# Optimization experiments

Hardware: AMD Instinct MI355X
Metric: run time of the kernel (lower is better)

Reference implementation:

```python
import jax, jax.numpy as jnp
import numpy as np

D_K = 64
NEG_INF = -1.0e9


def setup_inputs() -> dict:
    key = jax.random.key(0)
    kq, kk, kv = jax.random.split(key, 3)
    B, H, S, D = 2, 16, 2048, D_K
    Q = jax.random.normal(kq, (B, H, S, D), dtype=jnp.float32)
    K = jax.random.normal(kk, (B, H, S, D), dtype=jnp.float32)
    V = jax.random.normal(kv, (B, H, S, D), dtype=jnp.float32)
    # causal mask: True where attention is DISALLOWED (strict upper triangle)
    attn_mask = jnp.triu(jnp.ones((S, S), dtype=bool), k=1)
    return {"Q": Q, "K": K, "V": V, "attn_mask": attn_mask}


def reference(Q, K, V, attn_mask):
    # scores = Q @ (K / sqrt(d_k))^T  -> [B,H,S,S]
    scale = 1.0 / np.sqrt(D_K).astype(np.float32)
    scores = jnp.einsum("bhqd,bhkd->bhqk", Q, K * scale)
    scores = jnp.where(attn_mask, NEG_INF, scores)  # masked_fill_(mask, -1e9)
    attn = jax.nn.softmax(scores, axis=-1)
    context = jnp.einsum("bhqk,bhkd->bhqd", attn, V)
    return (context, attn)
```

## Files before the change

### kernel.cpp

```cpp
#include <hip/hip_runtime.h>

constexpr int S_LEN = 2048;
constexpr int D_K   = 64;
constexpr int N_BH  = 32;
constexpr int KB    = 64;
constexpr int PLP   = 80;

typedef __attribute__((ext_vector_type(8))) short short8;
typedef __attribute__((ext_vector_type(4))) float f32x4;
typedef unsigned short ushort_t;

__device__ __forceinline__ unsigned short f2bf(float f) {
    unsigned int u = __builtin_bit_cast(unsigned int, f);
    u += 0x7fffu + ((u >> 16) & 1u);
    return (unsigned short)(u >> 16);
}
__device__ __forceinline__ float bf2f(unsigned short h) {
    unsigned int u = ((unsigned int)h) << 16;
    return __builtin_bit_cast(float, u);
}

__global__ __launch_bounds__(256)
void prep_k(const float* __restrict__ K, ushort_t* __restrict__ Kws) {
    const int idx = blockIdx.x * 256 + threadIdx.x;
    const float4* src = (const float4*)K + (size_t)idx * 2;
    float4 a = src[0], b = src[1];
    float x[8] = {a.x, a.y, a.z, a.w, b.x, b.y, b.z, b.w};
    short8 o;
    #pragma unroll
    for (int j = 0; j < 8; ++j) o[j] = (short)f2bf(x[j] * 0.125f);
    *(short8*)(Kws + (size_t)idx * 8) = o;
}

__global__ __launch_bounds__(256)
void prep_v(const float* __restrict__ V, ushort_t* __restrict__ Vws) {
    const int gid = blockIdx.x * 256 + threadIdx.x;
    const int u   = gid & 511;
    const int bc  = gid >> 9;
    const int c   = bc & 31;
    const int bh  = bc >> 5;
    const int kg  = u >> 6;
    const int d   = u & 63;
    const float* vp = V + ((size_t)bh * S_LEN + c * KB + kg * 8) * D_K + d;
    short8 o;
    #pragma unroll
    for (int i = 0; i < 8; ++i) o[i] = (short)f2bf(vp[(size_t)i * D_K]);
    *(short8*)(Vws + ((size_t)(bh * 32 + c) * D_K + d) * KB + kg * 8) = o;
}

__global__ __launch_bounds__(512, 4)
void sdpa_main(const float* __restrict__ Q, const ushort_t* __restrict__ Kws,
               const ushort_t* __restrict__ Vws, float* __restrict__ out)
{
    __shared__ __align__(16) ushort_t Kbuf[2][4096];
    __shared__ __align__(16) ushort_t Vbuf[2][4096];
    __shared__ __align__(16) ushort_t Plds[8][16 * PLP];

    const int tid = threadIdx.x;
    const int w   = tid >> 6;
    const int l   = tid & 63;
    const int lr  = l & 15;
    const int lh  = l >> 4;

    const int b    = blockIdx.x;
    const int s    = b >> 8;
    const int cidx = b & 255;
    const int rmap = cidx & 7;
    const int bh   = cidx >> 3;
    const int qblk = s ? (15 - rmap) : rmap;
    const int q0   = qblk * 128;
    const int qw   = q0 + w * 16;
    const int nch  = 2 * (qblk + 1);

    float* ctx_out  = out;
    float* attn_out = out + (size_t)N_BH * S_LEN * D_K;

    short8 qhi[2], qlo[2];
    {
        const float* qrow = Q + ((size_t)bh * S_LEN + qw + lr) * D_K;
        #pragma unroll
        for (int ds = 0; ds < 2; ++ds) {
            const float4* p4 = (const float4*)(qrow + ds * 32 + lh * 8);
            float4 a = p4[0], bq = p4[1];
            float x[8] = {a.x, a.y, a.z, a.w, bq.x, bq.y, bq.z, bq.w};
            short8 hi, lo;
            #pragma unroll
            for (int j = 0; j < 8; ++j) {
                unsigned short h = f2bf(x[j]);
                hi[j] = (short)h;
                lo[j] = (short)f2bf(x[j] - bf2f(h));
            }
            qhi[ds] = hi; qlo[ds] = lo;
        }
    }

    const short8* Kt  = (const short8*)(Kws + (size_t)bh * S_LEN * D_K);
    const short8* Vt8 = (const short8*)(Vws + (size_t)bh * 32 * 4096);

    const int wrow  = tid >> 3;
    const int wcol  = (tid & 7) << 4;
    const int wphys = wrow * 128 + (wcol ^ ((wrow & 7) << 4));

    const int rsw = (lr & 7) << 4;

    float inv_[4];
    {
        float sum[4] = {0.f, 0.f, 0.f, 0.f};
        short8 kst = Kt[tid];
        *(short8*)((char*)&Kbuf[0][0] + wphys) = kst;
        __syncthreads();
        for (int c = 0; c < nch; ++c) {
            if (c + 1 < nch) kst = Kt[(c + 1) * 512 + tid];
            const char* Kb = (const char*)&Kbuf[c & 1][0];
            #pragma unroll
            for (int nt = 0; nt < 4; ++nt) {
                f32x4 acc = {0.f, 0.f, 0.f, 0.f};
                #pragma unroll
                for (int ks = 0; ks < 2; ++ks) {
                    short8 bk = *(const short8*)(Kb + (nt * 16 + lr) * 128 + ((ks * 64 + lh * 16) ^ rsw));
                    acc = __builtin_amdgcn_mfma_f32_16x16x32_bf16(qhi[ks], bk, acc, 0, 0, 0);
                    acc = __builtin_amdgcn_mfma_f32_16x16x32_bf16(qlo[ks], bk, acc, 0, 0, 0);
                }
                const int kg = c * KB + nt * 16 + lr;
                #pragma unroll
                for (int rr = 0; rr < 4; ++rr) {
                    if (kg <= qw + lh * 4 + rr)
                        sum[rr] += __expf(fminf(acc[rr], 60.f));
                }
            }
            if (c + 1 < nch) *(short8*)((char*)&Kbuf[(c + 1) & 1][0] + wphys) = kst;
            __syncthreads();
        }
        #pragma unroll
        for (int rr = 0; rr < 4; ++rr) {
            float t = sum[rr];
            t += __shfl_xor(t, 1);
            t += __shfl_xor(t, 2);
            t += __shfl_xor(t, 4);
            t += __shfl_xor(t, 8);
            inv_[rr] = 1.f / t;
        }
    }

    f32x4 ctx[4];
    #pragma unroll
    for (int nt = 0; nt < 4; ++nt) ctx[nt] = (f32x4){0.f, 0.f, 0.f, 0.f};

    {
        short8 kst = Kt[tid], vst = Vt8[tid];
        *(short8*)((char*)&Kbuf[0][0] + wphys) = kst;
        *(short8*)((char*)&Vbuf[0][0] + wphys) = vst;
        __syncthreads();
        for (int c = 0; c < nch; ++c) {
            if (c + 1 < nch) {
                kst = Kt[(c + 1) * 512 + tid];
                vst = Vt8[(c + 1) * 512 + tid];
            }
            const char* Kb = (const char*)&Kbuf[c & 1][0];
            const char* Vb = (const char*)&Vbuf[c & 1][0];

            #pragma unroll
            for (int nt = 0; nt < 4; ++nt) {
                f32x4 acc = {0.f, 0.f, 0.f, 0.f};
                #pragma unroll
                for (int ks = 0; ks < 2; ++ks) {
                    short8 bk = *(const short8*)(Kb + (nt * 16 + lr) * 128 + ((ks * 64 + lh * 16) ^ rsw));
                    acc = __builtin_amdgcn_mfma_f32_16x16x32_bf16(qhi[ks], bk, acc, 0, 0, 0);
                    acc = __builtin_amdgcn_mfma_f32_16x16x32_bf16(qlo[ks], bk, acc, 0, 0, 0);
                }
                const int kg = c * KB + nt * 16 + lr;
                #pragma unroll
                for (int rr = 0; rr < 4; ++rr) {
                    const int qg = qw + lh * 4 + rr;
                    float p = (kg <= qg) ? __expf(fminf(acc[rr], 60.f)) * inv_[rr] : 0.f;
                    attn_out[((size_t)bh * S_LEN + qg) * S_LEN + kg] = p;
                    Plds[w][(lh * 4 + rr) * PLP + nt * 16 + lr] = f2bf(p);
                }
            }

            #pragma unroll
            for (int ks = 0; ks < 2; ++ks) {
                short8 pa = *(const short8*)&Plds[w][lr * PLP + ks * 32 + lh * 8];
                #pragma unroll
                for (int nt = 0; nt < 4; ++nt) {
                    short8 vb = *(const short8*)(Vb + (nt * 16 + lr) * 128 + ((ks * 64 + lh * 16) ^ rsw));
                    ctx[nt] = __builtin_amdgcn_mfma_f32_16x16x32_bf16(pa, vb, ctx[nt], 0, 0, 0);
                }
            }

            if (c + 1 < nch) {
                *(short8*)((char*)&Kbuf[(c + 1) & 1][0] + wphys) = kst;
                *(short8*)((char*)&Vbuf[(c + 1) & 1][0] + wphys) = vst;
            }
            __syncthreads();
        }
    }

    #pragma unroll
    for (int nt = 0; nt < 4; ++nt)
        #pragma unroll
        for (int rr = 0; rr < 4; ++rr)
            ctx_out[((size_t)bh * S_LEN + qw + lh * 4 + rr) * D_K + nt * 16 + lr] = ctx[nt][rr];

    const int k0 = nch * KB;
    if (k0 < S_LEN) {
        const float4 z = {0.f, 0.f, 0.f, 0.f};
        for (int rr = 0; rr < 128; ++rr) {
            float* rowp = attn_out + ((size_t)bh * S_LEN + q0 + rr) * S_LEN;
            for (int k = k0 + tid * 4; k < S_LEN; k += 512 * 4)
                *(float4*)(rowp + k) = z;
        }
    }
}

constexpr int LDP = 72;

__global__ __launch_bounds__(256)
void sdpa_fused_v1(const float* __restrict__ Q, const float* __restrict__ K,
                   const float* __restrict__ V, float* __restrict__ out)
{
    __shared__ __align__(16) unsigned short Klds[KB * LDP];
    __shared__ __align__(16) unsigned short Vtlds[D_K * LDP];
    __shared__ __align__(16) unsigned short Pl[4][16 * LDP];

    const int tid = threadIdx.x;
    const int w   = tid >> 6;
    const int l   = tid & 63;
    const int lr  = l & 15;
    const int lh  = l >> 4;

    const int bh   = blockIdx.y;
    const int qblk = (int)gridDim.x - 1 - (int)blockIdx.x;
    const int q0   = qblk * 64;
    const int qw   = q0 + w * 16;
    const int nchunks = qblk + 1;

    const size_t in_base = (size_t)bh * S_LEN * D_K;
    float* ctx_out  = out;
    float* attn_out = out + (size_t)N_BH * S_LEN * D_K;

    short8 qhi[2], qlo[2];
    {
        const float* qrow = Q + in_base + (size_t)(qw + lr) * D_K;
        #pragma unroll
        for (int ds = 0; ds < 2; ++ds) {
            const float4* p4 = (const float4*)(qrow + ds * 32 + lh * 8);
            float4 a = p4[0], b = p4[1];
            float x[8] = {a.x, a.y, a.z, a.w, b.x, b.y, b.z, b.w};
            short8 hi, lo;
            #pragma unroll
            for (int j = 0; j < 8; ++j) {
                unsigned short h = f2bf(x[j]);
                hi[j] = (short)h;
                lo[j] = (short)f2bf(x[j] - bf2f(h));
            }
            qhi[ds] = hi; qlo[ds] = lo;
        }
    }

    const int srow = tid >> 2;
    const int scol = (tid & 3) * 16;
    const float* kstage = K + in_base + (size_t)srow * D_K + scol;
    const float* vstage = V + in_base + (size_t)srow * D_K + scol;

    float inv_[4];
    {
        float sum[4] = {0.f, 0.f, 0.f, 0.f};
        for (int c = 0; c < nchunks; ++c) {
            {
                const float4* kp = (const float4*)(kstage + (size_t)c * KB * D_K);
                float4 a0 = kp[0], a1 = kp[1], a2 = kp[2], a3 = kp[3];
                float x[16] = {a0.x,a0.y,a0.z,a0.w, a1.x,a1.y,a1.z,a1.w,
                               a2.x,a2.y,a2.z,a2.w, a3.x,a3.y,a3.z,a3.w};
                short8 w0, w1;
                #pragma unroll
                for (int j = 0; j < 8; ++j) {
                    w0[j] = (short)f2bf(x[j]     * 0.125f);
                    w1[j] = (short)f2bf(x[j + 8] * 0.125f);
                }
                *(short8*)&Klds[srow * LDP + scol]     = w0;
                *(short8*)&Klds[srow * LDP + scol + 8] = w1;
            }
            __syncthreads();
            #pragma unroll
            for (int nt = 0; nt < 4; ++nt) {
                f32x4 acc = {0.f, 0.f, 0.f, 0.f};
                #pragma unroll
                for (int ks = 0; ks < 2; ++ks) {
                    short8 bk = *(const short8*)&Klds[(nt*16 + lr) * LDP + ks*32 + lh*8];
                    acc = __builtin_amdgcn_mfma_f32_16x16x32_bf16(qhi[ks], bk, acc, 0, 0, 0);
                    acc = __builtin_amdgcn_mfma_f32_16x16x32_bf16(qlo[ks], bk, acc, 0, 0, 0);
                }
                const int kg = c * KB + nt * 16 + lr;
                #pragma unroll
                for (int rr = 0; rr < 4; ++rr) {
                    if (kg <= qw + lh * 4 + rr)
                        sum[rr] += __expf(fminf(acc[rr], 60.f));
                }
            }
            __syncthreads();
        }
        #pragma unroll
        for (int rr = 0; rr < 4; ++rr) {
            float t = sum[rr];
            t += __shfl_xor(t, 1);
            t += __shfl_xor(t, 2);
            t += __shfl_xor(t, 4);
            t += __shfl_xor(t, 8);
            inv_[rr] = 1.f / t;
        }
    }

    f32x4 ctx[4];
    #pragma unroll
    for (int nt = 0; nt < 4; ++nt) ctx[nt] = (f32x4){0.f, 0.f, 0.f, 0.f};

    for (int c = 0; c < nchunks; ++c) {
        {
            const float4* kp = (const float4*)(kstage + (size_t)c * KB * D_K);
            float4 a0 = kp[0], a1 = kp[1], a2 = kp[2], a3 = kp[3];
            float x[16] = {a0.x,a0.y,a0.z,a0.w, a1.x,a1.y,a1.z,a1.w,
                           a2.x,a2.y,a2.z,a2.w, a3.x,a3.y,a3.z,a3.w};
            short8 w0, w1;
            #pragma unroll
            for (int j = 0; j < 8; ++j) {
                w0[j] = (short)f2bf(x[j]     * 0.125f);
                w1[j] = (short)f2bf(x[j + 8] * 0.125f);
            }
            *(short8*)&Klds[srow * LDP + scol]     = w0;
            *(short8*)&Klds[srow * LDP + scol + 8] = w1;

            const float4* vp = (const float4*)(vstage + (size_t)c * KB * D_K);
            float4 b0 = vp[0], b1 = vp[1], b2 = vp[2], b3 = vp[3];
            float y[16] = {b0.x,b0.y,b0.z,b0.w, b1.x,b1.y,b1.z,b1.w,
                           b2.x,b2.y,b2.z,b2.w, b3.x,b3.y,b3.z,b3.w};
            #pragma unroll
            for (int j = 0; j < 16; ++j)
                Vtlds[(scol + j) * LDP + srow] = f2bf(y[j]);
        }
        __syncthreads();

        #pragma unroll
        for (int nt = 0; nt < 4; ++nt) {
            f32x4 acc = {0.f, 0.f, 0.f, 0.f};
            #pragma unroll
            for (int ks = 0; ks < 2; ++ks) {
                short8 bk = *(const short8*)&Klds[(nt*16 + lr) * LDP + ks*32 + lh*8];
                acc = __builtin_amdgcn_mfma_f32_16x16x32_bf16(qhi[ks], bk, acc, 0, 0, 0);
                acc = __builtin_amdgcn_mfma_f32_16x16x32_bf16(qlo[ks], bk, acc, 0, 0, 0);
            }
            const int kg = c * KB + nt * 16 + lr;
            #pragma unroll
            for (int rr = 0; rr < 4; ++rr) {
                const int qg = qw + lh * 4 + rr;
                float p = (kg <= qg) ? __expf(fminf(acc[rr], 60.f)) * inv_[rr] : 0.f;
                attn_out[((size_t)bh * S_LEN + qg) * S_LEN + kg] = p;
                Pl[w][(lh * 4 + rr) * LDP + nt * 16 + lr] = f2bf(p);
            }
        }
        __syncthreads();

        #pragma unroll
        for (int ks = 0; ks < 2; ++ks) {
            short8 pa = *(const short8*)&Pl[w][lr * LDP + ks*32 + lh*8];
            #pragma unroll
            for (int nt = 0; nt < 4; ++nt) {
                short8 vb = *(const short8*)&Vtlds[(nt*16 + lr) * LDP + ks*32 + lh*8];
                ctx[nt] = __builtin_amdgcn_mfma_f32_16x16x32_bf16(pa, vb, ctx[nt], 0, 0, 0);
            }
        }
        __syncthreads();
    }

    #pragma unroll
    for (int nt = 0; nt < 4; ++nt)
        #pragma unroll
        for (int rr = 0; rr < 4; ++rr)
            ctx_out[((size_t)bh * S_LEN + qw + lh * 4 + rr) * D_K + nt * 16 + lr] = ctx[nt][rr];

    const int k0 = nchunks * KB;
    if (k0 < S_LEN) {
        const float4 z = {0.f, 0.f, 0.f, 0.f};
        for (int rr = 0; rr < 64; ++rr) {
            float* rowp = attn_out + ((size_t)bh * S_LEN + q0 + rr) * S_LEN;
            for (int k = k0 + tid * 4; k < S_LEN; k += 256 * 4)
                *(float4*)(rowp + k) = z;
        }
    }
}

extern "C" void kernel_launch(void* const* d_in, const int* in_sizes, int n_in,
                              void* d_out, int out_size, void* d_ws, size_t ws_size,
                              hipStream_t stream)
{
    const float* Q = (const float*)d_in[0];
    const float* K = (const float*)d_in[1];
    const float* V = (const float*)d_in[2];
    float* out = (float*)d_out;

    const size_t ws_needed = (size_t)2 * N_BH * S_LEN * D_K * sizeof(ushort_t);
    if (ws_size >= ws_needed) {
        ushort_t* Kws = (ushort_t*)d_ws;
        ushort_t* Vws = Kws + (size_t)N_BH * S_LEN * D_K;
        prep_k<<<2048, 256, 0, stream>>>(K, Kws);
        prep_v<<<2048, 256, 0, stream>>>(V, Vws);
        sdpa_main<<<512, 512, 0, stream>>>(Q, Kws, Vws, out);
    } else {
        dim3 grid(S_LEN / 64, N_BH);
        sdpa_fused_v1<<<grid, 256, 0, stream>>>(Q, K, V, out);
    }
}
```

Baseline: 193.4 us.

## Coalesce attention-probability stores via swizzled LDS staging and unroll chunk loops by two

Each chunk's probabilities are now written only to a per-wave, XOR-swizzled LDS tile. They are read back row-wise and written to the attention output as contiguous float4 stores, replacing the scattered per-element global stores. Both K/V chunk loops are unrolled by two with fixed buffer indices and two chunks prefetched into registers. s_setprio is raised around the MFMA sections. The risks: the attention output is now rebuilt from bf16-rounded values, which costs precision, and the enlarged Plds array raises LDS use per block, which may lower occupancy.

```diff
diff --git a/kernel.cpp b/kernel.cpp
--- a/kernel.cpp
+++ b/kernel.cpp
@@ -4,7 +4,6 @@
 constexpr int D_K   = 64;
 constexpr int N_BH  = 32;
 constexpr int KB    = 64;
-constexpr int PLP   = 80;
 
 typedef __attribute__((ext_vector_type(8))) short short8;
 typedef __attribute__((ext_vector_type(4))) float f32x4;
@@ -54,7 +53,7 @@
 {
     __shared__ __align__(16) ushort_t Kbuf[2][4096];
     __shared__ __align__(16) ushort_t Vbuf[2][4096];
-    __shared__ __align__(16) ushort_t Plds[8][16 * PLP];
+    __shared__ __align__(16) ushort_t Plds[8][2048];
 
     const int tid = threadIdx.x;
     const int w   = tid >> 6;
@@ -100,18 +99,15 @@
     const int wrow  = tid >> 3;
     const int wcol  = (tid & 7) << 4;
     const int wphys = wrow * 128 + (wcol ^ ((wrow & 7) << 4));
-
-    const int rsw = (lr & 7) << 4;
+    const int rsw   = (lr & 7) << 4;
 
     float inv_[4];
     {
         float sum[4] = {0.f, 0.f, 0.f, 0.f};
-        short8 kst = Kt[tid];
-        *(short8*)((char*)&Kbuf[0][0] + wphys) = kst;
-        __syncthreads();
-        for (int c = 0; c < nch; ++c) {
-            if (c + 1 < nch) kst = Kt[(c + 1) * 512 + tid];
-            const char* Kb = (const char*)&Kbuf[c & 1][0];
+
+        auto p1 = [&](const ushort_t* Kbp, int c) {
+            const char* Kb = (const char*)Kbp;
+            __builtin_amdgcn_s_setprio(1);
             #pragma unroll
             for (int nt = 0; nt < 4; ++nt) {
                 f32x4 acc = {0.f, 0.f, 0.f, 0.f};
@@ -128,7 +124,21 @@
                         sum[rr] += __expf(fminf(acc[rr], 60.f));
                 }
             }
-            if (c + 1 < nch) *(short8*)((char*)&Kbuf[(c + 1) & 1][0] + wphys) = kst;
+            __builtin_amdgcn_s_setprio(0);
+        };
+
+        short8 kA = Kt[tid];
+        short8 kB = Kt[512 + tid];
+        *(short8*)((char*)&Kbuf[0][0] + wphys) = kA;
+        __syncthreads();
+        for (int c = 0; c < nch; c += 2) {
+            if (c + 2 < nch) kA = Kt[(c + 2) * 512 + tid];
+            p1(&Kbuf[0][0], c);
+            *(short8*)((char*)&Kbuf[1][0] + wphys) = kB;
+            __syncthreads();
+            if (c + 3 < nch) kB = Kt[(c + 3) * 512 + tid];
+            p1(&Kbuf[1][0], c + 1);
+            if (c + 2 < nch) *(short8*)((char*)&Kbuf[0][0] + wphys) = kA;
             __syncthreads();
         }
         #pragma unroll
@@ -146,51 +156,73 @@
     #pragma unroll
     for (int nt = 0; nt < 4; ++nt) ctx[nt] = (f32x4){0.f, 0.f, 0.f, 0.f};
 
+    const int sqr = l >> 2;
+    const int sm  = l & 3;
+    float* srowp = attn_out + ((size_t)bh * S_LEN + qw + sqr) * S_LEN;
+
     {
-        short8 kst = Kt[tid], vst = Vt8[tid];
-        *(short8*)((char*)&Kbuf[0][0] + wphys) = kst;
-        *(short8*)((char*)&Vbuf[0][0] + wphys) = vst;
-        __syncthreads();
-        for (int c = 0; c < nch; ++c) {
-            if (c + 1 < nch) {
-                kst = Kt[(c + 1) * 512 + tid];
-                vst = Vt8[(c + 1) * 512 + tid];
-            }
-            const char* Kb = (const char*)&Kbuf[c & 1][0];
-            const char* Vb = (const char*)&Vbuf[c & 1][0];
-
+        auto p2 = [&](const ushort_t* Kbp, const ushort_t* Vbp, int c) {
+            const char* Kb = (const char*)Kbp;
+            const char* Vb = (const char*)Vbp;
             #pragma unroll
             for (int nt = 0; nt < 4; ++nt) {
                 f32x4 acc = {0.f, 0.f, 0.f, 0.f};
+                __builtin_amdgcn_s_setprio(1);
                 #pragma unroll
                 for (int ks = 0; ks < 2; ++ks) {
                     short8 bk = *(const short8*)(Kb + (nt * 16 + lr) * 128 + ((ks * 64 + lh * 16) ^ rsw));
                     acc = __builtin_amdgcn_mfma_f32_16x16x32_bf16(qhi[ks], bk, acc, 0, 0, 0);
                     acc = __builtin_amdgcn_mfma_f32_16x16x32_bf16(qlo[ks], bk, acc, 0, 0, 0);
                 }
+                __builtin_amdgcn_s_setprio(0);
                 const int kg = c * KB + nt * 16 + lr;
                 #pragma unroll
                 for (int rr = 0; rr < 4; ++rr) {
-                    const int qg = qw + lh * 4 + rr;
+                    const int pwr = lh * 4 + rr;
+                    const int qg  = qw + pwr;
                     float p = (kg <= qg) ? __expf(fminf(acc[rr], 60.f)) * inv_[rr] : 0.f;
-                    attn_out[((size_t)bh * S_LEN + qg) * S_LEN + kg] = p;
-                    Plds[w][(lh * 4 + rr) * PLP + nt * 16 + lr] = f2bf(p);
-                }
-            }
-
+                    Plds[w][pwr * 64 + ((nt * 16 + lr) ^ ((pwr & 7) << 3))] = f2bf(p);
+                }
+            }
+            __builtin_amdgcn_s_setprio(1);
             #pragma unroll
             for (int ks = 0; ks < 2; ++ks) {
-                short8 pa = *(const short8*)&Plds[w][lr * PLP + ks * 32 + lh * 8];
+                short8 pa = *(const short8*)&Plds[w][lr * 64 + ((ks * 32 + lh * 8) ^ ((lr & 7) << 3))];
                 #pragma unroll
                 for (int nt = 0; nt < 4; ++nt) {
                     short8 vb = *(const short8*)(Vb + (nt * 16 + lr) * 128 + ((ks * 64 + lh * 16) ^ rsw));
                     ctx[nt] = __builtin_amdgcn_mfma_f32_16x16x32_bf16(pa, vb, ctx[nt], 0, 0, 0);
                 }
             }
-
-            if (c + 1 < nch) {
-                *(short8*)((char*)&Kbuf[(c + 1) & 1][0] + wphys) = kst;
-                *(short8*)((char*)&Vbuf[(c + 1) & 1][0] + wphys) = vst;
+            __builtin_amdgcn_s_setprio(0);
+            #pragma unroll
+            for (int j = 0; j < 2; ++j) {
+                short8 pv = *(const short8*)&Plds[w][sqr * 64 + ((sm * 16 + j * 8) ^ ((sqr & 7) << 3))];
+                float f[8];
+                #pragma unroll
+                for (int e = 0; e < 8; ++e) f[e] = bf2f((ushort_t)pv[e]);
+                float* dst = srowp + c * KB + sm * 16 + j * 8;
+                *(float4*)(dst)     = (float4){f[0], f[1], f[2], f[3]};
+                *(float4*)(dst + 4) = (float4){f[4], f[5], f[6], f[7]};
+            }
+        };
+
+        short8 kA = Kt[tid],        vA = Vt8[tid];
+        short8 kB = Kt[512 + tid],  vB = Vt8[512 + tid];
+        *(short8*)((char*)&Kbuf[0][0] + wphys) = kA;
+        *(short8*)((char*)&Vbuf[0][0] + wphys) = vA;
+        __syncthreads();
+        for (int c = 0; c < nch; c += 2) {
+            if (c + 2 < nch) { kA = Kt[(c + 2) * 512 + tid]; vA = Vt8[(c + 2) * 512 + tid]; }
+            p2(&Kbuf[0][0], &Vbuf[0][0], c);
+            *(short8*)((char*)&Kbuf[1][0] + wphys) = kB;
+            *(short8*)((char*)&Vbuf[1][0] + wphys) = vB;
+            __syncthreads();
+            if (c + 3 < nch) { kB = Kt[(c + 3) * 512 + tid]; vB = Vt8[(c + 3) * 512 + tid]; }
+            p2(&Kbuf[1][0], &Vbuf[1][0], c + 1);
+            if (c + 2 < nch) {
+                *(short8*)((char*)&Kbuf[0][0] + wphys) = kA;
+                *(short8*)((char*)&Vbuf[0][0] + wphys) = vA;
             }
             __syncthreads();
         }
```

Result: slower. 214.4 us (+10.8%).

## Split query tile across wave pairs and pair causal tiles per block

Applied to the files above, without the earlier changes.

Each block now processes two 64-row query tiles, one long (31-r) and one short (r), for balanced causal work per block. The 8 waves are split into 4 query groups times 2 key-column halves, so each wave computes half the score columns and the row sums are combined through a small shared-memory reduction. P is exchanged across wave pairs via a swizzled shared buffer before the PV MFMA, and the masked-zero fill is reorganised per row. This adds extra barriers and cross-wave reductions in exchange for load balance and fewer per-wave registers.

```diff
diff --git a/kernel.cpp b/kernel.cpp
--- a/kernel.cpp
+++ b/kernel.cpp
@@ -4,7 +4,6 @@
 constexpr int D_K   = 64;
 constexpr int N_BH  = 32;
 constexpr int KB    = 64;
-constexpr int PLP   = 80;
 
 typedef __attribute__((ext_vector_type(8))) short short8;
 typedef __attribute__((ext_vector_type(4))) float f32x4;
@@ -54,45 +53,23 @@
 {
     __shared__ __align__(16) ushort_t Kbuf[2][4096];
     __shared__ __align__(16) ushort_t Vbuf[2][4096];
-    __shared__ __align__(16) ushort_t Plds[8][16 * PLP];
+    __shared__ __align__(16) ushort_t Plds[8][1024];
+    __shared__ float sred[2][4][16];
 
     const int tid = threadIdx.x;
     const int w   = tid >> 6;
     const int l   = tid & 63;
     const int lr  = l & 15;
     const int lh  = l >> 4;
-
-    const int b    = blockIdx.x;
-    const int s    = b >> 8;
-    const int cidx = b & 255;
-    const int rmap = cidx & 7;
-    const int bh   = cidx >> 3;
-    const int qblk = s ? (15 - rmap) : rmap;
-    const int q0   = qblk * 128;
-    const int qw   = q0 + w * 16;
-    const int nch  = 2 * (qblk + 1);
+    const int g   = w & 3;
+    const int h2  = w >> 2;
+
+    const int bx = blockIdx.x;
+    const int bh = bx >> 4;
+    const int r  = bx & 15;
 
     float* ctx_out  = out;
     float* attn_out = out + (size_t)N_BH * S_LEN * D_K;
-
-    short8 qhi[2], qlo[2];
-    {
-        const float* qrow = Q + ((size_t)bh * S_LEN + qw + lr) * D_K;
-        #pragma unroll
-        for (int ds = 0; ds < 2; ++ds) {
-            const float4* p4 = (const float4*)(qrow + ds * 32 + lh * 8);
-            float4 a = p4[0], bq = p4[1];
-            float x[8] = {a.x, a.y, a.z, a.w, bq.x, bq.y, bq.z, bq.w};
-            short8 hi, lo;
-            #pragma unroll
-            for (int j = 0; j < 8; ++j) {
-                unsigned short h = f2bf(x[j]);
-                hi[j] = (short)h;
-                lo[j] = (short)f2bf(x[j] - bf2f(h));
-            }
-            qhi[ds] = hi; qlo[ds] = lo;
-        }
-    }
 
     const short8* Kt  = (const short8*)(Kws + (size_t)bh * S_LEN * D_K);
     const short8* Vt8 = (const short8*)(Vws + (size_t)bh * 32 * 4096);
@@ -100,117 +77,152 @@
     const int wrow  = tid >> 3;
     const int wcol  = (tid & 7) << 4;
     const int wphys = wrow * 128 + (wcol ^ ((wrow & 7) << 4));
-
-    const int rsw = (lr & 7) << 4;
-
-    float inv_[4];
-    {
-        float sum[4] = {0.f, 0.f, 0.f, 0.f};
-        short8 kst = Kt[tid];
-        *(short8*)((char*)&Kbuf[0][0] + wphys) = kst;
-        __syncthreads();
-        for (int c = 0; c < nch; ++c) {
-            if (c + 1 < nch) kst = Kt[(c + 1) * 512 + tid];
-            const char* Kb = (const char*)&Kbuf[c & 1][0];
-            #pragma unroll
-            for (int nt = 0; nt < 4; ++nt) {
-                f32x4 acc = {0.f, 0.f, 0.f, 0.f};
+    const int rsw   = (lr & 7) << 4;
+
+    auto run_tile = [&](int qt0, int nch) {
+        short8 qhi[2], qlo[2];
+        {
+            const float* qrow = Q + ((size_t)bh * S_LEN + qt0 + g * 16 + lr) * D_K;
+            #pragma unroll
+            for (int ds = 0; ds < 2; ++ds) {
+                const float4* p4 = (const float4*)(qrow + ds * 32 + lh * 8);
+                float4 a = p4[0], bq = p4[1];
+                float x[8] = {a.x, a.y, a.z, a.w, bq.x, bq.y, bq.z, bq.w};
+                short8 hi, lo;
+                #pragma unroll
+                for (int j = 0; j < 8; ++j) {
+                    unsigned short h = f2bf(x[j]);
+                    hi[j] = (short)h;
+                    lo[j] = (short)f2bf(x[j] - bf2f(h));
+                }
+                qhi[ds] = hi; qlo[ds] = lo;
+            }
+        }
+        const int qg_base = qt0 + g * 16 + lh * 4;
+
+        float inv_[4];
+        {
+            float sum[4] = {0.f, 0.f, 0.f, 0.f};
+            short8 kst = Kt[tid];
+            *(short8*)((char*)&Kbuf[0][0] + wphys) = kst;
+            __syncthreads();
+            for (int c = 0; c < nch; ++c) {
+                if (c + 1 < nch) kst = Kt[(c + 1) * 512 + tid];
+                const char* Kb = (const char*)&Kbuf[c & 1][0];
+                #pragma unroll
+                for (int nt2 = 0; nt2 < 2; ++nt2) {
+                    const int ntg = h2 * 2 + nt2;
+                    f32x4 acc = {0.f, 0.f, 0.f, 0.f};
+                    #pragma unroll
+                    for (int ks = 0; ks < 2; ++ks) {
+                        short8 bk = *(const short8*)(Kb + (ntg * 16 + lr) * 128 + ((ks * 64 + lh * 16) ^ rsw));
+                        acc = __builtin_amdgcn_mfma_f32_16x16x32_bf16(qhi[ks], bk, acc, 0, 0, 0);
+                        acc = __builtin_amdgcn_mfma_f32_16x16x32_bf16(qlo[ks], bk, acc, 0, 0, 0);
+                    }
+                    const int kg = c * KB + ntg * 16 + lr;
+                    #pragma unroll
+                    for (int rr = 0; rr < 4; ++rr) {
+                        if (kg <= qg_base + rr)
+                            sum[rr] += __expf(fminf(acc[rr], 60.f));
+                    }
+                }
+                if (c + 1 < nch) *(short8*)((char*)&Kbuf[(c + 1) & 1][0] + wphys) = kst;
+                __syncthreads();
+            }
+            #pragma unroll
+            for (int rr = 0; rr < 4; ++rr) {
+                float t = sum[rr];
+                t += __shfl_xor(t, 1);
+                t += __shfl_xor(t, 2);
+                t += __shfl_xor(t, 4);
+                t += __shfl_xor(t, 8);
+                sum[rr] = t;
+            }
+            if (lr == 0) {
+                #pragma unroll
+                for (int rr = 0; rr < 4; ++rr) sred[h2][g][lh * 4 + rr] = sum[rr];
+            }
+            __syncthreads();
+            #pragma unroll
+            for (int rr = 0; rr < 4; ++rr)
+                inv_[rr] = 1.f / (sred[0][g][lh * 4 + rr] + sred[1][g][lh * 4 + rr]);
+            __syncthreads();
+        }
+
+        f32x4 ctx[2];
+        ctx[0] = (f32x4){0.f, 0.f, 0.f, 0.f};
+        ctx[1] = (f32x4){0.f, 0.f, 0.f, 0.f};
+
+        {
+            short8 kst = Kt[tid], vst = Vt8[tid];
+            *(short8*)((char*)&Kbuf[0][0] + wphys) = kst;
+            *(short8*)((char*)&Vbuf[0][0] + wphys) = vst;
+            __syncthreads();
+            for (int c = 0; c < nch; ++c) {
+                if (c + 1 < nch) { kst = Kt[(c + 1) * 512 + tid]; vst = Vt8[(c + 1) * 512 + tid]; }
+                const char* Kb = (const char*)&Kbuf[c & 1][0];
+                const char* Vb = (const char*)&Vbuf[c & 1][0];
+
+                #pragma unroll
+                for (int nt2 = 0; nt2 < 2; ++nt2) {
+                    const int ntg = h2 * 2 + nt2;
+                    f32x4 acc = {0.f, 0.f, 0.f, 0.f};
+                    #pragma unroll
+                    for (int ks = 0; ks < 2; ++ks) {
+                        short8 bk = *(const short8*)(Kb + (ntg * 16 + lr) * 128 + ((ks * 64 + lh * 16) ^ rsw));
+                        acc = __builtin_amdgcn_mfma_f32_16x16x32_bf16(qhi[ks], bk, acc, 0, 0, 0);
+                        acc = __builtin_amdgcn_mfma_f32_16x16x32_bf16(qlo[ks], bk, acc, 0, 0, 0);
+                    }
+                    const int kg = c * KB + ntg * 16 + lr;
+                    #pragma unroll
+                    for (int rr = 0; rr < 4; ++rr) {
+                        const int pwr = lh * 4 + rr;
+                        const int qg  = qg_base + rr;
+                        float p = (kg <= qg) ? __expf(fminf(acc[rr], 60.f)) * inv_[rr] : 0.f;
+                        attn_out[((size_t)bh * S_LEN + qg) * S_LEN + kg] = p;
+                        Plds[g + 4 * h2][pwr * 64 + ((ntg * 16 + lr) ^ ((pwr & 7) << 3))] = f2bf(p);
+                    }
+                }
+                __syncthreads();
+
                 #pragma unroll
                 for (int ks = 0; ks < 2; ++ks) {
-                    short8 bk = *(const short8*)(Kb + (nt * 16 + lr) * 128 + ((ks * 64 + lh * 16) ^ rsw));
-                    acc = __builtin_amdgcn_mfma_f32_16x16x32_bf16(qhi[ks], bk, acc, 0, 0, 0);
-                    acc = __builtin_amdgcn_mfma_f32_16x16x32_bf16(qlo[ks], bk, acc, 0, 0, 0);
-                }
-                const int kg = c * KB + nt * 16 + lr;
-                #pragma unroll
-                for (int rr = 0; rr < 4; ++rr) {
-                    if (kg <= qw + lh * 4 + rr)
-                        sum[rr] += __expf(fminf(acc[rr], 60.f));
-                }
-            }
-            if (c + 1 < nch) *(short8*)((char*)&Kbuf[(c + 1) & 1][0] + wphys) = kst;
-            __syncthreads();
-        }
-        #pragma unroll
-        for (int rr = 0; rr < 4; ++rr) {
-            float t = sum[rr];
-            t += __shfl_xor(t, 1);
-            t += __shfl_xor(t, 2);
-            t += __shfl_xor(t, 4);
-            t += __shfl_xor(t, 8);
-            inv_[rr] = 1.f / t;
-        }
-    }
-
-    f32x4 ctx[4];
-    #pragma unroll
-    for (int nt = 0; nt < 4; ++nt) ctx[nt] = (f32x4){0.f, 0.f, 0.f, 0.f};
-
-    {
-        short8 kst = Kt[tid], vst = Vt8[tid];
-        *(short8*)((char*)&Kbuf[0][0] + wphys) = kst;
-        *(short8*)((char*)&Vbuf[0][0] + wphys) = vst;
-        __syncthreads();
-        for (int c = 0; c < nch; ++c) {
-            if (c + 1 < nch) {
-                kst = Kt[(c + 1) * 512 + tid];
-                vst = Vt8[(c + 1) * 512 + tid];
-            }
-            const char* Kb = (const char*)&Kbuf[c & 1][0];
-            const char* Vb = (const char*)&Vbuf[c & 1][0];
-
-            #pragma unroll
-            for (int nt = 0; nt < 4; ++nt) {
-                f32x4 acc = {0.f, 0.f, 0.f, 0.f};
-                #pragma unroll
-                for (int ks = 0; ks < 2; ++ks) {
-                    short8 bk = *(const short8*)(Kb + (nt * 16 + lr) * 128 + ((ks * 64 + lh * 16) ^ rsw));
-                    acc = __builtin_amdgcn_mfma_f32_16x16x32_bf16(qhi[ks], bk, acc, 0, 0, 0);
-                    acc = __builtin_amdgcn_mfma_f32_16x16x32_bf16(qlo[ks], bk, acc, 0, 0, 0);
-                }
-                const int kg = c * KB + nt * 16 + lr;
-                #pragma unroll
-                for (int rr = 0; rr < 4; ++rr) {
-                    const int qg = qw + lh * 4 + rr;
-                    float p = (kg <= qg) ? __expf(fminf(acc[rr], 60.f)) * inv_[rr] : 0.f;
-                    attn_out[((size_t)bh * S_LEN + qg) * S_LEN + kg] = p;
-                    Plds[w][(lh * 4 + rr) * PLP + nt * 16 + lr] = f2bf(p);
-                }
-            }
-
-            #pragma unroll
-            for (int ks = 0; ks < 2; ++ks) {
-                short8 pa = *(const short8*)&Plds[w][lr * PLP + ks * 32 + lh * 8];
-                #pragma unroll
-                for (int nt = 0; nt < 4; ++nt) {
-                    short8 vb = *(const short8*)(Vb + (nt * 16 + lr) * 128 + ((ks * 64 + lh * 16) ^ rsw));
-                    ctx[nt] = __builtin_amdgcn_mfma_f32_16x16x32_bf16(pa, vb, ctx[nt], 0, 0, 0);
-                }
-            }
-
-            if (c + 1 < nch) {
-                *(short8*)((char*)&Kbuf[(c + 1) & 1][0] + wphys) = kst;
-                *(short8*)((char*)&Vbuf[(c + 1) & 1][0] + wphys) = vst;
-            }
-            __syncthreads();
-        }
-    }
-
-    #pragma unroll
-    for (int nt = 0; nt < 4; ++nt)
-        #pragma unroll
-        for (int rr = 0; rr < 4; ++rr)
-            ctx_out[((size_t)bh * S_LEN + qw + lh * 4 + rr) * D_K + nt * 16 + lr] = ctx[nt][rr];
-
-    const int k0 = nch * KB;
-    if (k0 < S_LEN) {
-        const float4 z = {0.f, 0.f, 0.f, 0.f};
-        for (int rr = 0; rr < 128; ++rr) {
-            float* rowp = attn_out + ((size_t)bh * S_LEN + q0 + rr) * S_LEN;
-            for (int k = k0 + tid * 4; k < S_LEN; k += 512 * 4)
+                    short8 pa = *(const short8*)&Plds[g + 4 * ks][lr * 64 + ((ks * 32 + lh * 8) ^ ((lr & 7) << 3))];
+                    #pragma unroll
+                    for (int nt2 = 0; nt2 < 2; ++nt2) {
+                        const int ntg = h2 * 2 + nt2;
+                        short8 vb = *(const short8*)(Vb + (ntg * 16 + lr) * 128 + ((ks * 64 + lh * 16) ^ rsw));
+                        ctx[nt2] = __builtin_amdgcn_mfma_f32_16x16x32_bf16(pa, vb, ctx[nt2], 0, 0, 0);
+                    }
+                }
+
+                if (c + 1 < nch) {
+                    *(short8*)((char*)&Kbuf[(c + 1) & 1][0] + wphys) = kst;
+                    *(short8*)((char*)&Vbuf[(c + 1) & 1][0] + wphys) = vst;
+                }
+                __syncthreads();
+            }
+        }
+
+        #pragma unroll
+        for (int nt2 = 0; nt2 < 2; ++nt2) {
+            const int ntg = h2 * 2 + nt2;
+            #pragma unroll
+            for (int rr = 0; rr < 4; ++rr)
+                ctx_out[((size_t)bh * S_LEN + qg_base + rr) * D_K + ntg * 16 + lr] = ctx[nt2][rr];
+        }
+
+        const int k0 = nch * KB;
+        if (k0 < S_LEN) {
+            const float4 z = {0.f, 0.f, 0.f, 0.f};
+            float* rowp = attn_out + ((size_t)bh * S_LEN + qt0 + (tid >> 3)) * S_LEN;
+            for (int k = k0 + (tid & 7) * 4; k < S_LEN; k += 32)
                 *(float4*)(rowp + k) = z;
         }
-    }
+    };
+
+    run_tile((31 - r) * 64, 32 - r);
+    run_tile(r * 64, r + 1);
 }
 
 constexpr int LDP = 72;
```

Result: faster. 188.1 us (-2.7%).

## Pair complementary causal query tiles per block to balance work and share K/V loads

Applied to the files above, without the earlier changes.

Each 512-thread block now handles two 64-row query tiles from opposite ends of the causal triangle (r and 31-r), with the two wave halves sharing the same K/V chunk stream. This makes every block process 33 chunks of work, balancing load across blocks instead of having blocks with 2 to 32 chunks. It also XOR-swizzles the P staging buffer in LDS instead of padding it, and restructures the zero-fill of the masked upper triangle. In exchange, the short-tile waves sit idle at barriers while the long-tile waves finish the remaining chunks.

```diff
diff --git a/kernel.cpp b/kernel.cpp
--- a/kernel.cpp
+++ b/kernel.cpp
@@ -4,7 +4,6 @@
 constexpr int D_K   = 64;
 constexpr int N_BH  = 32;
 constexpr int KB    = 64;
-constexpr int PLP   = 80;
 
 typedef __attribute__((ext_vector_type(8))) short short8;
 typedef __attribute__((ext_vector_type(4))) float f32x4;
@@ -54,30 +53,43 @@
 {
     __shared__ __align__(16) ushort_t Kbuf[2][4096];
     __shared__ __align__(16) ushort_t Vbuf[2][4096];
-    __shared__ __align__(16) ushort_t Plds[8][16 * PLP];
-
-    const int tid = threadIdx.x;
-    const int w   = tid >> 6;
-    const int l   = tid & 63;
-    const int lr  = l & 15;
-    const int lh  = l >> 4;
-
-    const int b    = blockIdx.x;
-    const int s    = b >> 8;
-    const int cidx = b & 255;
-    const int rmap = cidx & 7;
-    const int bh   = cidx >> 3;
-    const int qblk = s ? (15 - rmap) : rmap;
-    const int q0   = qblk * 128;
-    const int qw   = q0 + w * 16;
-    const int nch  = 2 * (qblk + 1);
+    __shared__ __align__(16) ushort_t Plds[8][1024];
+
+    const int tid  = threadIdx.x;
+    const int w    = tid >> 6;
+    const int l    = tid & 63;
+    const int lr   = l & 15;
+    const int lh   = l >> 4;
+    const int g    = w & 3;
+    const int half = w >> 2;
+
+    const int b  = blockIdx.x;
+    const int s  = b >> 8;
+    const int i  = b & 255;
+    const int bh = (i >> 4) + s * 16;
+    const int r0 = i & 15;
+    const int r  = s ? (15 - r0) : r0;
+
+    const int nchA  = 32 - r;
+    const int nchB  = r + 1;
+    const int q0    = (half ? r : (31 - r)) * 64;
+    const int mynch = half ? nchB : nchA;
+    const int qg_base = q0 + g * 16 + lh * 4;
 
     float* ctx_out  = out;
     float* attn_out = out + (size_t)N_BH * S_LEN * D_K;
 
+    const short8* Kt  = (const short8*)(Kws + (size_t)bh * S_LEN * D_K);
+    const short8* Vt8 = (const short8*)(Vws + (size_t)bh * 32 * 4096);
+
+    const int wrow  = tid >> 3;
+    const int wcol  = (tid & 7) << 4;
+    const int wphys = wrow * 128 + (wcol ^ ((wrow & 7) << 4));
+    const int rsw   = (lr & 7) << 4;
+
     short8 qhi[2], qlo[2];
     {
-        const float* qrow = Q + ((size_t)bh * S_LEN + qw + lr) * D_K;
+        const float* qrow = Q + ((size_t)bh * S_LEN + q0 + g * 16 + lr) * D_K;
         #pragma unroll
         for (int ds = 0; ds < 2; ++ds) {
             const float4* p4 = (const float4*)(qrow + ds * 32 + lh * 8);
@@ -94,24 +106,11 @@
         }
     }
 
-    const short8* Kt  = (const short8*)(Kws + (size_t)bh * S_LEN * D_K);
-    const short8* Vt8 = (const short8*)(Vws + (size_t)bh * 32 * 4096);
-
-    const int wrow  = tid >> 3;
-    const int wcol  = (tid & 7) << 4;
-    const int wphys = wrow * 128 + (wcol ^ ((wrow & 7) << 4));
-
-    const int rsw = (lr & 7) << 4;
-
     float inv_[4];
     {
         float sum[4] = {0.f, 0.f, 0.f, 0.f};
-        short8 kst = Kt[tid];
-        *(short8*)((char*)&Kbuf[0][0] + wphys) = kst;
-        __syncthreads();
-        for (int c = 0; c < nch; ++c) {
-            if (c + 1 < nch) kst = Kt[(c + 1) * 512 + tid];
-            const char* Kb = (const char*)&Kbuf[c & 1][0];
+
+        auto qk_sum = [&](const char* Kb, int c) {
             #pragma unroll
             for (int nt = 0; nt < 4; ++nt) {
                 f32x4 acc = {0.f, 0.f, 0.f, 0.f};
@@ -123,13 +122,26 @@
                 }
                 const int kg = c * KB + nt * 16 + lr;
                 #pragma unroll
-                for (int rr = 0; rr < 4; ++rr) {
-                    if (kg <= qw + lh * 4 + rr)
-                        sum[rr] += __expf(fminf(acc[rr], 60.f));
-                }
-            }
-            if (c + 1 < nch) *(short8*)((char*)&Kbuf[(c + 1) & 1][0] + wphys) = kst;
+                for (int rr = 0; rr < 4; ++rr)
+                    if (kg <= qg_base + rr) sum[rr] += __expf(fminf(acc[rr], 60.f));
+            }
+        };
+
+        short8 kE = Kt[tid];
+        *(short8*)((char*)&Kbuf[0][0] + wphys) = kE;
+        short8 kO = Kt[512 + tid];
+        __syncthreads();
+        for (int c = 0; c < nchA; c += 2) {
+            if (c + 2 < nchA) kE = Kt[(c + 2) * 512 + tid];
+            if (c < mynch) qk_sum((const char*)&Kbuf[0][0], c);
+            if (c + 1 < nchA) *(short8*)((char*)&Kbuf[1][0] + wphys) = kO;
             __syncthreads();
+            if (c + 1 < nchA) {
+                if (c + 3 < nchA) kO = Kt[(c + 3) * 512 + tid];
+                if (c + 1 < mynch) qk_sum((const char*)&Kbuf[1][0], c + 1);
+                if (c + 2 < nchA) *(short8*)((char*)&Kbuf[0][0] + wphys) = kE;
+                __syncthreads();
+            }
         }
         #pragma unroll
         for (int rr = 0; rr < 4; ++rr) {
@@ -147,18 +159,7 @@
     for (int nt = 0; nt < 4; ++nt) ctx[nt] = (f32x4){0.f, 0.f, 0.f, 0.f};
 
     {
-        short8 kst = Kt[tid], vst = Vt8[tid];
-        *(short8*)((char*)&Kbuf[0][0] + wphys) = kst;
-        *(short8*)((char*)&Vbuf[0][0] + wphys) = vst;
-        __syncthreads();
-        for (int c = 0; c < nch; ++c) {
-            if (c + 1 < nch) {
-                kst = Kt[(c + 1) * 512 + tid];
-                vst = Vt8[(c + 1) * 512 + tid];
-            }
-            const char* Kb = (const char*)&Kbuf[c & 1][0];
-            const char* Vb = (const char*)&Vbuf[c & 1][0];
-
+        auto p2 = [&](const char* Kb, const char* Vb, int c) {
             #pragma unroll
             for (int nt = 0; nt < 4; ++nt) {
                 f32x4 acc = {0.f, 0.f, 0.f, 0.f};
@@ -171,28 +172,46 @@
                 const int kg = c * KB + nt * 16 + lr;
                 #pragma unroll
                 for (int rr = 0; rr < 4; ++rr) {
-                    const int qg = qw + lh * 4 + rr;
+                    const int pwr = lh * 4 + rr;
+                    const int qg  = qg_base + rr;
                     float p = (kg <= qg) ? __expf(fminf(acc[rr], 60.f)) * inv_[rr] : 0.f;
                     attn_out[((size_t)bh * S_LEN + qg) * S_LEN + kg] = p;
-                    Plds[w][(lh * 4 + rr) * PLP + nt * 16 + lr] = f2bf(p);
-                }
-            }
-
+                    Plds[w][pwr * 64 + ((nt * 16 + lr) ^ ((pwr & 7) << 3))] = f2bf(p);
+                }
+            }
             #pragma unroll
             for (int ks = 0; ks < 2; ++ks) {
-                short8 pa = *(const short8*)&Plds[w][lr * PLP + ks * 32 + lh * 8];
+                short8 pa = *(const short8*)&Plds[w][lr * 64 + ((ks * 32 + lh * 8) ^ ((lr & 7) << 3))];
                 #pragma unroll
                 for (int nt = 0; nt < 4; ++nt) {
                     short8 vb = *(const short8*)(Vb + (nt * 16 + lr) * 128 + ((ks * 64 + lh * 16) ^ rsw));
                     ctx[nt] = __builtin_amdgcn_mfma_f32_16x16x32_bf16(pa, vb, ctx[nt], 0, 0, 0);
                 }
             }
-
-            if (c + 1 < nch) {
-                *(short8*)((char*)&Kbuf[(c + 1) & 1][0] + wphys) = kst;
-                *(short8*)((char*)&Vbuf[(c + 1) & 1][0] + wphys) = vst;
+        };
+
+        short8 kE = Kt[tid],        vE = Vt8[tid];
+        *(short8*)((char*)&Kbuf[0][0] + wphys) = kE;
+        *(short8*)((char*)&Vbuf[0][0] + wphys) = vE;
+        short8 kO = Kt[512 + tid],  vO = Vt8[512 + tid];
+        __syncthreads();
+        for (int c = 0; c < nchA; c += 2) {
+            if (c + 2 < nchA) { kE = Kt[(c + 2) * 512 + tid]; vE = Vt8[(c + 2) * 512 + tid]; }
+            if (c < mynch) p2((const char*)&Kbuf[0][0], (const char*)&Vbuf[0][0], c);
+            if (c + 1 < nchA) {
+                *(short8*)((char*)&Kbuf[1][0] + wphys) = kO;
+                *(short8*)((char*)&Vbuf[1][0] + wphys) = vO;
             }
             __syncthreads();
+            if (c + 1 < nchA) {
+                if (c + 3 < nchA) { kO = Kt[(c + 3) * 512 + tid]; vO = Vt8[(c + 3) * 512 + tid]; }
+                if (c + 1 < mynch) p2((const char*)&Kbuf[1][0], (const char*)&Vbuf[1][0], c + 1);
+                if (c + 2 < nchA) {
+                    *(short8*)((char*)&Kbuf[0][0] + wphys) = kE;
+                    *(short8*)((char*)&Vbuf[0][0] + wphys) = vE;
+                }
+                __syncthreads();
+            }
         }
     }
 
@@ -200,16 +219,18 @@
     for (int nt = 0; nt < 4; ++nt)
         #pragma unroll
         for (int rr = 0; rr < 4; ++rr)
-            ctx_out[((size_t)bh * S_LEN + qw + lh * 4 + rr) * D_K + nt * 16 + lr] = ctx[nt][rr];
-
-    const int k0 = nch * KB;
-    if (k0 < S_LEN) {
+            ctx_out[((size_t)bh * S_LEN + qg_base + rr) * D_K + nt * 16 + lr] = ctx[nt][rr];
+
+    {
         const float4 z = {0.f, 0.f, 0.f, 0.f};
-        for (int rr = 0; rr < 128; ++rr) {
-            float* rowp = attn_out + ((size_t)bh * S_LEN + q0 + rr) * S_LEN;
-            for (int k = k0 + tid * 4; k < S_LEN; k += 512 * 4)
-                *(float4*)(rowp + k) = z;
-        }
+        const int rowa = (31 - r) * 64 + (tid >> 3);
+        float* rpa = attn_out + ((size_t)bh * S_LEN + rowa) * S_LEN;
+        for (int k = nchA * KB + (tid & 7) * 4; k < S_LEN; k += 32)
+            *(float4*)(rpa + k) = z;
+        const int rowb = r * 64 + (tid >> 3);
+        float* rpb = attn_out + ((size_t)bh * S_LEN + rowb) * S_LEN;
+        for (int k = nchB * KB + (tid & 7) * 4; k < S_LEN; k += 32)
+            *(float4*)(rpb + k) = z;
     }
 }
 
```

New measurement: 182.3 us. 5.7% less time.
